# Kernel optimization log

Hardware: AMD Instinct MI355X
Metric: run time of the kernel (lower is better)

The kernel has to match this reference:

```python
import jax, jax.numpy as jnp
import numpy as np

N_HEADS = 16
ROPE = 64        # qk_rope_head_dim
KV_LORA = 512
V_DIM = 128
THETA = 10000.0

def rms_norm(x, w, eps=1e-6):
    return x * jax.lax.rsqrt(jnp.mean(x * x, axis=-1, keepdims=True) + eps) * w

def rope_cos_sin(T, d, theta=THETA):
    half = d // 2
    inv = 1.0 / theta ** (jnp.arange(half, dtype=jnp.float32) / half)
    ang = jnp.arange(T, dtype=jnp.float32)[:, None] * inv  # (T, half)
    return jnp.cos(ang), jnp.sin(ang)

def apply_rot(x, cos, sin):
    # x: (B,T,H,D); complex rotation on interleaved pairs
    xr, xi = x[..., 0::2], x[..., 1::2]
    c = cos[None, :, None, :]
    s = sin[None, :, None, :]
    orr = xr * c - xi * s
    oi = xr * s + xi * c
    return jnp.stack([orr, oi], axis=-1).reshape(x.shape)

def setup_inputs() -> dict:
    key = jax.random.key(0)
    ks = jax.random.split(key, 8)
    B, T, C = 2, 2048, 2048
    QLR = 1536
    x = jax.random.normal(ks[0], (B, T, C), dtype=jnp.float32)
    mask = jnp.tril(jnp.ones((T, T), dtype=jnp.int32))[None, None]
    sc = 0.02
    w_qa = jax.random.normal(ks[1], (QLR, C), dtype=jnp.float32) * sc
    qa_norm_w = jnp.ones((QLR,), dtype=jnp.float32)
    w_qb = jax.random.normal(ks[2], (N_HEADS * 2 * ROPE, QLR), dtype=jnp.float32) * sc
    w_kva = jax.random.normal(ks[3], (KV_LORA + ROPE, C), dtype=jnp.float32) * sc
    kva_norm_w = jnp.ones((KV_LORA,), dtype=jnp.float32)
    w_kvb = jax.random.normal(ks[4], (N_HEADS * (ROPE + V_DIM), KV_LORA), dtype=jnp.float32) * sc
    w_o = jax.random.normal(ks[5], (C, N_HEADS * V_DIM), dtype=jnp.float32) * sc
    return {"x": x, "mask": mask, "w_qa": w_qa, "qa_norm_w": qa_norm_w, "w_qb": w_qb,
            "w_kva": w_kva, "kva_norm_w": kva_norm_w, "w_kvb": w_kvb, "w_o": w_o}

def reference(x, mask, w_qa, qa_norm_w, w_qb, w_kva, kva_norm_w, w_kvb, w_o):
    B, T, C = x.shape
    # Q: low-rank compress -> norm -> up-project, split nope/rope halves
    q_c = rms_norm(x @ w_qa.T, qa_norm_w)
    q = (q_c @ w_qb.T).reshape(B, T, N_HEADS, 2 * ROPE)
    q_nope, q_rope = q[..., :ROPE], q[..., ROPE:]
    # KV: joint low-rank + shared rope key
    kv_a = x @ w_kva.T
    kv_c = rms_norm(kv_a[..., :KV_LORA], kva_norm_w)
    k_rope_raw = kv_a[..., KV_LORA:]                       # (B,T,ROPE)
    kv = (kv_c @ w_kvb.T).reshape(B, T, N_HEADS, ROPE + V_DIM)
    k_content, v = kv[..., :ROPE], kv[..., ROPE:]
    k_rope = jnp.broadcast_to(k_rope_raw[:, :, None, :], (B, T, N_HEADS, ROPE))
    cos, sin = rope_cos_sin(T, ROPE)
    q_rope = apply_rot(q_rope, cos, sin)
    k_rope = apply_rot(k_rope, cos, sin)
    q = jnp.concatenate([q_nope, q_rope], axis=-1)         # (B,T,H,2*ROPE)
    k = jnp.concatenate([k_content, k_rope], axis=-1)
    att = jnp.einsum('bqhd,bkhd->bhqk', q, k) * (ROPE ** -0.5)
    att = jnp.where(mask == 0, -jnp.inf, att)
    att = jax.nn.softmax(att, axis=-1)
    # source's nan-guard: uniform attention if any nan appeared
    att = jnp.where(jnp.any(jnp.isnan(att)), jnp.float32(1.0 / T), att)
    out = jnp.einsum('bhqk,bkhd->bqhd', att, v).reshape(B, T, N_HEADS * V_DIM)
    return out @ w_o.T
```

## Files before the change

kernel.cpp:

```cpp
#include <hip/hip_runtime.h>

typedef short bf16x8 __attribute__((ext_vector_type(8)));
typedef unsigned short u16x8 __attribute__((ext_vector_type(8)));
typedef unsigned short u16x4 __attribute__((ext_vector_type(4)));
typedef float f32x4 __attribute__((ext_vector_type(4)));
typedef unsigned u32x4 __attribute__((ext_vector_type(4)));
typedef unsigned u32x2 __attribute__((ext_vector_type(2)));

#define DEV static __device__ __forceinline__

DEV float bf2f(unsigned short u) { return __uint_as_float(((unsigned)u) << 16); }
DEV unsigned short f2bf(float f) {
  unsigned u = __float_as_uint(f);
  return (unsigned short)((u + 0x7fffu + ((u >> 16) & 1u)) >> 16);
}
DEV unsigned cvtpk(float lo, float hi) {
  unsigned r;
  asm("v_cvt_pk_bf16_f32 %0, %1, %2" : "=v"(r) : "v"(lo), "v"(hi));
  return r;
}
DEV void p32swap(unsigned& a, unsigned& b) {
  asm volatile("v_permlane32_swap_b32 %0, %1" : "+v"(a), "+v"(b));
}
DEV void p16swap(unsigned& a, unsigned& b) {
  asm volatile("v_permlane16_swap_b32 %0, %1" : "+v"(a), "+v"(b));
}

#define GLDS16(g, l)                                                                   \
  __builtin_amdgcn_global_load_lds((const __attribute__((address_space(1))) void*)(g), \
                                   (__attribute__((address_space(3))) void*)(l), 16, 0, 0)

__global__ __launch_bounds__(256) void convert_pad(const float* __restrict__ src,
                                                   unsigned short* __restrict__ dst,
                                                   int rows, int cols, int dstRows) {
  int i = blockIdx.x * 256 + threadIdx.x;
  int total4 = (dstRows * cols) >> 2;
  if (i >= total4) return;
  int e = i << 2;
  int r = e / cols;
  int c = e - r * cols;
  u16x4 o = {0, 0, 0, 0};
  if (r < rows) {
    const float* p = src + (size_t)r * cols + c;
    o[0] = f2bf(p[0]); o[1] = f2bf(p[1]); o[2] = f2bf(p[2]); o[3] = f2bf(p[3]);
  }
  *(u16x4*)(dst + e) = o;
}

template <typename OutT>
__global__ __launch_bounds__(256, 2) void gemm_bt(const unsigned short* __restrict__ A,
                                                  const unsigned short* __restrict__ B,
                                                  OutT* __restrict__ C, int M, int N, int K) {
  __shared__ __align__(16) unsigned short As[128 * 64];
  __shared__ __align__(16) unsigned short Bs[128 * 64];
  const int tid = threadIdx.x;
  const int lane = tid & 63, wave = tid >> 6;
  const int l16 = lane & 15, lhi = lane >> 4;
  const int nbn = N >> 7;
  const int bm = blockIdx.x / nbn, bn = blockIdx.x - bm * nbn;
  const int m0 = bm << 7, n0 = bn << 7;
  const int wm = (wave >> 1) << 6, wn = (wave & 1) << 6;
  f32x4 acc[4][4] = {};
  for (int k0 = 0; k0 < K; k0 += 64) {
#pragma unroll
    for (int it = 0; it < 4; ++it) {
      int slot = it * 256 + tid;
      int row = slot >> 3, col = (slot & 7) << 3;
      GLDS16(A + (size_t)(m0 + row) * K + k0 + col, As + (it * 256 + wave * 64) * 8);
      GLDS16(B + (size_t)(n0 + row) * K + k0 + col, Bs + (it * 256 + wave * 64) * 8);
    }
    __syncthreads();
#pragma unroll
    for (int ks = 0; ks < 2; ++ks) {
      bf16x8 a[4], b[4];
#pragma unroll
      for (int i = 0; i < 4; ++i) {
        a[i] = *(const bf16x8*)(As + (wm + i * 16 + l16) * 64 + ks * 32 + lhi * 8);
        b[i] = *(const bf16x8*)(Bs + (wn + i * 16 + l16) * 64 + ks * 32 + lhi * 8);
      }
#pragma unroll
      for (int i = 0; i < 4; ++i)
#pragma unroll
        for (int j = 0; j < 4; ++j)
          acc[i][j] = __builtin_amdgcn_mfma_f32_16x16x32_bf16(a[i], b[j], acc[i][j], 0, 0, 0);
    }
    __syncthreads();
  }
#pragma unroll
  for (int i = 0; i < 4; ++i)
#pragma unroll
    for (int j = 0; j < 4; ++j)
#pragma unroll
      for (int r = 0; r < 4; ++r) {
        int row = m0 + wm + i * 16 + lhi * 4 + r;
        int col = n0 + wn + j * 16 + l16;
        float v = acc[i][j][r];
        if constexpr (sizeof(OutT) == 4)
          C[(size_t)row * N + col] = v;
        else
          C[(size_t)row * N + col] = (OutT)f2bf(v);
      }
}

__global__ __launch_bounds__(256) void rms_q(const unsigned short* __restrict__ in,
                                             const float* __restrict__ w,
                                             unsigned short* __restrict__ out) {
  const int row = blockIdx.x, tid = threadIdx.x;
  const unsigned short* p = in + (size_t)row * 2176;
  float f[8];
  float ss = 0.f;
  const bool act = tid < 192;
  if (act) {
    u16x8 v = *(const u16x8*)(p + tid * 8);
#pragma unroll
    for (int j = 0; j < 8; ++j) { f[j] = bf2f(v[j]); ss += f[j] * f[j]; }
  }
#pragma unroll
  for (int m = 1; m <= 32; m <<= 1) ss += __shfl_xor(ss, m);
  __shared__ float red[4];
  if ((tid & 63) == 0) red[tid >> 6] = ss;
  __syncthreads();
  float rstd = rsqrtf((red[0] + red[1] + red[2] + red[3]) * (1.f / 1536.f) + 1e-6f);
  if (act) {
    u16x8 o;
#pragma unroll
    for (int j = 0; j < 8; ++j) o[j] = f2bf(f[j] * rstd * w[tid * 8 + j]);
    *(u16x8*)(out + (size_t)row * 1536 + tid * 8) = o;
  }
}

__global__ __launch_bounds__(256) void rms_kv(const unsigned short* __restrict__ qkva,
                                              const float* __restrict__ w,
                                              unsigned short* __restrict__ kvc,
                                              unsigned short* __restrict__ krope) {
  const int row = blockIdx.x, tid = threadIdx.x;
  const unsigned short* p = qkva + (size_t)row * 2176 + 1536;
  float f0 = bf2f(p[tid * 2]), f1 = bf2f(p[tid * 2 + 1]);
  float ss = f0 * f0 + f1 * f1;
#pragma unroll
  for (int m = 1; m <= 32; m <<= 1) ss += __shfl_xor(ss, m);
  __shared__ float red[4];
  if ((tid & 63) == 0) red[tid >> 6] = ss;
  __syncthreads();
  float rstd = rsqrtf((red[0] + red[1] + red[2] + red[3]) * (1.f / 512.f) + 1e-6f);
  kvc[(size_t)row * 512 + tid * 2]     = f2bf(f0 * rstd * w[tid * 2]);
  kvc[(size_t)row * 512 + tid * 2 + 1] = f2bf(f1 * rstd * w[tid * 2 + 1]);
  if (tid < 32) {
    int j = tid;
    float xr = bf2f(p[512 + 2 * j]), xi = bf2f(p[512 + 2 * j + 1]);
    int t = row & 2047;
    float ang = (float)t * powf(10000.f, -(float)j * (1.f / 32.f));
    float c = cosf(ang), s = sinf(ang);
    krope[(size_t)row * 64 + 2 * j]     = f2bf(xr * c - xi * s);
    krope[(size_t)row * 64 + 2 * j + 1] = f2bf(xr * s + xi * c);
  }
}

__global__ __launch_bounds__(256) void kv_asm_k(const unsigned short* __restrict__ kvfull,
                                                const unsigned short* __restrict__ krope,
                                                unsigned short* __restrict__ K) {
  int i = blockIdx.x * 256 + threadIdx.x;
  if (i >= 2 * 2048 * 16 * 128) return;
  int d = i & 127, h = (i >> 7) & 15, tl = i >> 11;
  int b = tl >> 11, t = tl & 2047;
  size_t oidx = ((size_t)((b * 16 + h) * 2048 + t)) * 128 + d;
  K[oidx] = (d < 64) ? kvfull[(size_t)tl * 3072 + h * 192 + d] : krope[(size_t)tl * 64 + d - 64];
}

__global__ __launch_bounds__(256) void v_transpose(const unsigned short* __restrict__ kvfull,
                                                   unsigned short* __restrict__ VT) {
  __shared__ unsigned short tile[64][137];
  const int tid = threadIdx.x;
  const int tt = blockIdx.x & 31, h = (blockIdx.x >> 5) & 15, b = blockIdx.x >> 9;
  const int t0 = tt * 64;
#pragma unroll
  for (int it = 0; it < 4; ++it) {
    int s = it * 256 + tid;
    int r = s >> 4, c = (s & 15) << 3;
    u16x8 v = *(const u16x8*)(kvfull + (size_t)(b * 2048 + t0 + r) * 3072 + h * 192 + 64 + c);
    *(u16x8*)(&tile[r][c]) = v;
  }
  __syncthreads();
#pragma unroll
  for (int it = 0; it < 4; ++it) {
    int s = it * 256 + tid;
    int d = s >> 3, tc = (s & 7) << 3;
    u16x8 o;
#pragma unroll
    for (int j = 0; j < 8; ++j) o[j] = tile[tc + j][d];
    *(u16x8*)(VT + ((size_t)(b * 16 + h) * 128 + d) * 2048 + t0 + tc) = o;
  }
}

__global__ __launch_bounds__(256, 2) void flash_attn(const unsigned short* __restrict__ qfull,
                                                     const unsigned short* __restrict__ Kt,
                                                     const unsigned short* __restrict__ Vt,
                                                     unsigned short* __restrict__ out) {
  const int tid = threadIdx.x, lane = tid & 63, wave = tid >> 6;
  const int l16 = lane & 15, lhi = lane >> 4;
  const int pr = blockIdx.x & 15;
  const int h = (blockIdx.x >> 4) & 15;
  const int b = blockIdx.x >> 8;
  const int sA = pr, sB = 31 - pr;
  __shared__ __align__(16) unsigned short Ks[2][64 * 128];
  __shared__ __align__(16) unsigned short Vs[2][64 * 128];

  bf16x8 qf[2][4];
  float m_run[2], l_run[2];
  int qrow_g[2];
  f32x4 o_acc[2][8] = {};
#pragma unroll
  for (int u = 0; u < 2; ++u) {
    const int s_u = u ? sB : sA;
    int t = s_u * 64 + wave * 16 + l16;
    qrow_g[u] = t;
    const unsigned short* qrow = qfull + (size_t)(b * 2048 + t) * 2048 + h * 128;
#pragma unroll
    for (int ks = 0; ks < 4; ++ks) {
      u16x8 raw = *(const u16x8*)(qrow + ks * 32 + lhi * 8);
      float f[8];
#pragma unroll
      for (int j = 0; j < 8; ++j) f[j] = bf2f(raw[j]);
      if (ks >= 2) {
#pragma unroll
        for (int pp = 0; pp < 4; ++pp) {
          int d = ks * 32 + lhi * 8 + 2 * pp;
          int jl = (d - 64) >> 1;
          float ang = (float)t * powf(10000.f, -(float)jl * (1.f / 32.f));
          float c = cosf(ang), s = sinf(ang);
          float xr = f[2 * pp], xi = f[2 * pp + 1];
          f[2 * pp] = xr * c - xi * s;
          f[2 * pp + 1] = xr * s + xi * c;
        }
      }
      bf16x8 fr;
#pragma unroll
      for (int j = 0; j < 8; ++j) fr[j] = (short)f2bf(f[j] * 0.125f);
      qf[u][ks] = fr;
    }
    m_run[u] = -1e30f;
    l_run[u] = 0.f;
  }

  const unsigned short* Kbh = Kt + (size_t)(b * 16 + h) * 2048 * 128;
  const unsigned short* Vbh = Vt + (size_t)(b * 16 + h) * 128 * 2048;

  auto stageK = [&](int kt, int buf) {
#pragma unroll
    for (int it = 0; it < 4; ++it) {
      int L = it * 4096 + wave * 1024 + lane * 16;
      int r = L >> 8;
      int w = (L & 255) ^ ((r & 7) << 4);
      GLDS16(Kbh + (size_t)(kt * 64 + r) * 128 + (w >> 1), &Ks[buf][(it * 4096 + wave * 1024) >> 1]);
    }
  };
  auto stageV = [&](int kt, int buf) {
#pragma unroll
    for (int it = 0; it < 4; ++it) {
      int L = it * 4096 + wave * 1024 + lane * 16;
      int d = L >> 7;
      int w = (L & 127) ^ ((d & 7) << 4);
      GLDS16(Vbh + (size_t)d * 2048 + kt * 64 + (w >> 1), &Vs[buf][(it * 4096 + wave * 1024) >> 1]);
    }
  };

  stageK(0, 0);
  stageV(0, 0);
  __syncthreads();
  int cur = 0;

  for (int kt = 0; kt <= sB; ++kt) {
    if (kt < sB) { stageK(kt + 1, cur ^ 1); stageV(kt + 1, cur ^ 1); }
    const unsigned short* Kb = Ks[cur];
    const unsigned short* Vb = Vs[cur];
    const bool actA = (kt <= sA);

    f32x4 st[2][4] = {};
    __builtin_amdgcn_s_setprio(1);
#pragma unroll
    for (int ks = 0; ks < 4; ++ks) {
      bf16x8 kf[4];
#pragma unroll
      for (int nt = 0; nt < 4; ++nt) {
        int row = nt * 16 + l16;
        int byteoff = row * 256 + ((ks * 64 + lhi * 16) ^ ((l16 & 7) << 4));
        kf[nt] = *(const bf16x8*)((const char*)Kb + byteoff);
      }
#pragma unroll
      for (int u = 0; u < 2; ++u) {
        if (u == 0 && !actA) continue;
#pragma unroll
        for (int nt = 0; nt < 4; ++nt)
          st[u][nt] = __builtin_amdgcn_mfma_f32_16x16x32_bf16(kf[nt], qf[u][ks], st[u][nt], 0, 0, 0);
      }
    }
    __builtin_amdgcn_s_setprio(0);

    bf16x8 pw[2][2];
#pragma unroll
    for (int u = 0; u < 2; ++u) {
      if (u == 0 && !actA) continue;
      const int s_u = u ? sB : sA;
      if (kt == s_u) {
#pragma unroll
        for (int nt = 0; nt < 4; ++nt)
#pragma unroll
          for (int r = 0; r < 4; ++r) {
            int kg = kt * 64 + nt * 16 + lhi * 4 + r;
            st[u][nt][r] = (kg <= qrow_g[u]) ? st[u][nt][r] : -1e30f;
          }
      }
      float mx = -1e30f;
#pragma unroll
      for (int nt = 0; nt < 4; ++nt)
#pragma unroll
        for (int r = 0; r < 4; ++r) mx = fmaxf(mx, st[u][nt][r]);
      mx = fmaxf(mx, __shfl_xor(mx, 16));
      mx = fmaxf(mx, __shfl_xor(mx, 32));
      float mnew = fmaxf(m_run[u], mx);
      float sc = __expf(m_run[u] - mnew);
      m_run[u] = mnew;
      float sum = 0.f;
#pragma unroll
      for (int nt = 0; nt < 4; ++nt)
#pragma unroll
        for (int r = 0; r < 4; ++r) {
          float p = __expf(st[u][nt][r] - mnew);
          st[u][nt][r] = p;
          sum += p;
        }
      sum += __shfl_xor(sum, 16);
      sum += __shfl_xor(sum, 32);
      l_run[u] = l_run[u] * sc + sum;
#pragma unroll
      for (int dt = 0; dt < 8; ++dt) o_acc[u][dt] *= sc;
      unsigned pk01[4], pk23[4];
#pragma unroll
      for (int nt = 0; nt < 4; ++nt) {
        pk01[nt] = cvtpk(st[u][nt][0], st[u][nt][1]);
        pk23[nt] = cvtpk(st[u][nt][2], st[u][nt][3]);
      }
#pragma unroll
      for (int k2 = 0; k2 < 2; ++k2) {
        unsigned a0 = pk01[2 * k2], b0 = pk01[2 * k2 + 1];
        unsigned a1 = pk23[2 * k2], b1 = pk23[2 * k2 + 1];
        p32swap(a0, b0); p16swap(a0, b0);
        p32swap(a1, b1); p16swap(a1, b1);
        u32x4 t4 = {a0, a1, b0, b1};
        pw[u][k2] = *(bf16x8*)&t4;
      }
    }

    __builtin_amdgcn_s_setprio(1);
#pragma unroll
    for (int k2 = 0; k2 < 2; ++k2)
#pragma unroll
      for (int dt = 0; dt < 8; ++dt) {
        int row = dt * 16 + l16;
        int byteoff = row * 128 + ((k2 * 64 + lhi * 16) ^ ((l16 & 7) << 4));
        bf16x8 vf = *(const bf16x8*)((const char*)Vb + byteoff);
#pragma unroll
        for (int u = 0; u < 2; ++u) {
          if (u == 0 && !actA) continue;
          o_acc[u][dt] = __builtin_amdgcn_mfma_f32_16x16x32_bf16(vf, pw[u][k2], o_acc[u][dt], 0, 0, 0);
        }
      }
    __builtin_amdgcn_s_setprio(0);

    __syncthreads();
    cur ^= 1;
  }

#pragma unroll
  for (int u = 0; u < 2; ++u) {
    float inv = 1.0f / l_run[u];
    unsigned short* orow = out + (size_t)(b * 2048 + qrow_g[u]) * 2048 + h * 128;
#pragma unroll
    for (int dt = 0; dt < 8; ++dt) {
      unsigned w01 = cvtpk(o_acc[u][dt][0] * inv, o_acc[u][dt][1] * inv);
      unsigned w23 = cvtpk(o_acc[u][dt][2] * inv, o_acc[u][dt][3] * inv);
      u32x2 st2 = {w01, w23};
      *(u32x2*)(orow + dt * 16 + lhi * 4) = st2;
    }
  }
}

extern "C" void kernel_launch(void* const* d_in, const int* in_sizes, int n_in,
                              void* d_out, int out_size, void* d_ws, size_t ws_size,
                              hipStream_t stream) {
  (void)in_sizes; (void)n_in; (void)out_size; (void)ws_size;
  const float* x      = (const float*)d_in[0];
  const float* w_qa   = (const float*)d_in[2];
  const float* qa_nw  = (const float*)d_in[3];
  const float* w_qb   = (const float*)d_in[4];
  const float* w_kva  = (const float*)d_in[5];
  const float* kva_nw = (const float*)d_in[6];
  const float* w_kvb  = (const float*)d_in[7];
  const float* w_o    = (const float*)d_in[8];
  float* out = (float*)d_out;
  char* ws = (char*)d_ws;

  unsigned short* xb     = (unsigned short*)(ws + 0);
  unsigned short* wqkva  = (unsigned short*)(ws + 16777216);
  unsigned short* wqbb   = (unsigned short*)(ws + 25690112);
  unsigned short* wkvbb  = (unsigned short*)(ws + 31981568);
  unsigned short* wob    = (unsigned short*)(ws + 35127296);
  unsigned short* qkva   = (unsigned short*)(ws + 43515904);
  unsigned short* qfull  = (unsigned short*)(ws + 43515904);
  unsigned short* q_c    = (unsigned short*)(ws + 61341696);
  unsigned short* kv_c   = (unsigned short*)(ws + 73924608);
  unsigned short* krope  = (unsigned short*)(ws + 78118912);
  unsigned short* attno  = (unsigned short*)(ws + 61341696);
  unsigned short* Vattn  = (unsigned short*)(ws + 78643200);
  unsigned short* Kattn  = xb;
  unsigned short* kvfull = (unsigned short*)d_out;

  convert_pad<<<8192, 256, 0, stream>>>(x,     xb,    4096, 2048, 4096);
  convert_pad<<<3072, 256, 0, stream>>>(w_qa,  wqkva, 1536, 2048, 1536);
  convert_pad<<<1280, 256, 0, stream>>>(w_kva, wqkva + (size_t)1536 * 2048, 576, 2048, 640);
  convert_pad<<<3072, 256, 0, stream>>>(w_qb,  wqbb,  2048, 1536, 2048);
  convert_pad<<<1536, 256, 0, stream>>>(w_kvb, wkvbb, 3072,  512, 3072);
  convert_pad<<<4096, 256, 0, stream>>>(w_o,   wob,   2048, 2048, 2048);

  gemm_bt<unsigned short><<<32 * 17, 256, 0, stream>>>(xb, wqkva, qkva, 4096, 2176, 2048);

  rms_q<<<4096, 256, 0, stream>>>(qkva, qa_nw, q_c);
  rms_kv<<<4096, 256, 0, stream>>>(qkva, kva_nw, kv_c, krope);

  gemm_bt<unsigned short><<<32 * 16, 256, 0, stream>>>(q_c,  wqbb,  qfull,  4096, 2048, 1536);
  gemm_bt<unsigned short><<<32 * 24, 256, 0, stream>>>(kv_c, wkvbb, kvfull, 4096, 3072,  512);

  kv_asm_k<<<32768, 256, 0, stream>>>(kvfull, krope, Kattn);
  v_transpose<<<1024, 256, 0, stream>>>(kvfull, Vattn);

  flash_attn<<<512, 256, 0, stream>>>(qfull, Kattn, Vattn, attno);

  gemm_bt<float><<<32 * 16, 256, 0, stream>>>(attno, wob, out, 4096, 2048, 2048);
}
```

Baseline: 310.8 us.

## Fuse conversions and RMS norms, drop K assembly, add lazy softmax rescale

Merges the six fp32-to-bf16 conversion launches into one kernel and the two RMS-norm kernels into one. Removes the separate K-assembly kernel: flash attention now gathers K directly from the kv projection output and the rotated rope buffer during its LDS staging. Flash attention also folds log2(e) into the Q scale so it can use exp2f, skips the running-max rescale unless the max grows by more than 8, and remaps block indices so work is spread across XCDs. This cuts launches and an extra write and read of K, at the cost of strided gathers in the attention loads.

```diff
diff --git a/kernel.cpp b/kernel.cpp
--- a/kernel.cpp
+++ b/kernel.cpp
@@ -30,12 +30,9 @@
   __builtin_amdgcn_global_load_lds((const __attribute__((address_space(1))) void*)(g), \
                                    (__attribute__((address_space(3))) void*)(l), 16, 0, 0)
 
-__global__ __launch_bounds__(256) void convert_pad(const float* __restrict__ src,
-                                                   unsigned short* __restrict__ dst,
-                                                   int rows, int cols, int dstRows) {
-  int i = blockIdx.x * 256 + threadIdx.x;
-  int total4 = (dstRows * cols) >> 2;
-  if (i >= total4) return;
+DEV void cvt_body(const float* __restrict__ src, unsigned short* __restrict__ dst,
+                  int rows, int cols, int dstRows, int bid) {
+  int i = bid * 256 + (int)threadIdx.x;
   int e = i << 2;
   int r = e / cols;
   int c = e - r * cols;
@@ -45,6 +42,21 @@
     o[0] = f2bf(p[0]); o[1] = f2bf(p[1]); o[2] = f2bf(p[2]); o[3] = f2bf(p[3]);
   }
   *(u16x4*)(dst + e) = o;
+}
+
+__global__ __launch_bounds__(256) void convert_all(
+    const float* __restrict__ x, const float* __restrict__ w_qa, const float* __restrict__ w_kva,
+    const float* __restrict__ w_qb, const float* __restrict__ w_kvb, const float* __restrict__ w_o,
+    unsigned short* __restrict__ xb, unsigned short* __restrict__ wqkva,
+    unsigned short* __restrict__ wqbb, unsigned short* __restrict__ wkvbb,
+    unsigned short* __restrict__ wob) {
+  int bid = blockIdx.x;
+  if (bid < 8192)        cvt_body(x,     xb,                        4096, 2048, 4096, bid);
+  else if (bid < 11264)  cvt_body(w_qa,  wqkva,                     1536, 2048, 1536, bid - 8192);
+  else if (bid < 12544)  cvt_body(w_kva, wqkva + (size_t)1536*2048,  576, 2048,  640, bid - 11264);
+  else if (bid < 15616)  cvt_body(w_qb,  wqbb,                      2048, 1536, 2048, bid - 12544);
+  else if (bid < 17152)  cvt_body(w_kvb, wkvbb,                     3072,  512, 3072, bid - 15616);
+  else                   cvt_body(w_o,   wob,                       2048, 2048, 2048, bid - 17152);
 }
 
 template <typename OutT>
@@ -102,69 +114,51 @@
       }
 }
 
-__global__ __launch_bounds__(256) void rms_q(const unsigned short* __restrict__ in,
-                                             const float* __restrict__ w,
-                                             unsigned short* __restrict__ out) {
+__global__ __launch_bounds__(256) void rms_fused(const unsigned short* __restrict__ qkva,
+                                                 const float* __restrict__ qw,
+                                                 const float* __restrict__ kvw,
+                                                 unsigned short* __restrict__ q_c,
+                                                 unsigned short* __restrict__ kv_c,
+                                                 unsigned short* __restrict__ krope) {
   const int row = blockIdx.x, tid = threadIdx.x;
-  const unsigned short* p = in + (size_t)row * 2176;
-  float f[8];
-  float ss = 0.f;
+  const unsigned short* p = qkva + (size_t)row * 2176;
+  float fq[8];
+  float ssq = 0.f;
   const bool act = tid < 192;
   if (act) {
     u16x8 v = *(const u16x8*)(p + tid * 8);
 #pragma unroll
-    for (int j = 0; j < 8; ++j) { f[j] = bf2f(v[j]); ss += f[j] * f[j]; }
-  }
-#pragma unroll
-  for (int m = 1; m <= 32; m <<= 1) ss += __shfl_xor(ss, m);
-  __shared__ float red[4];
-  if ((tid & 63) == 0) red[tid >> 6] = ss;
+    for (int j = 0; j < 8; ++j) { fq[j] = bf2f(v[j]); ssq += fq[j] * fq[j]; }
+  }
+  float f0 = bf2f(p[1536 + tid * 2]), f1 = bf2f(p[1536 + tid * 2 + 1]);
+  float sskv = f0 * f0 + f1 * f1;
+#pragma unroll
+  for (int m = 1; m <= 32; m <<= 1) {
+    ssq += __shfl_xor(ssq, m);
+    sskv += __shfl_xor(sskv, m);
+  }
+  __shared__ float rq[4], rkv[4];
+  if ((tid & 63) == 0) { rq[tid >> 6] = ssq; rkv[tid >> 6] = sskv; }
   __syncthreads();
-  float rstd = rsqrtf((red[0] + red[1] + red[2] + red[3]) * (1.f / 1536.f) + 1e-6f);
+  float rstdq = rsqrtf((rq[0] + rq[1] + rq[2] + rq[3]) * (1.f / 1536.f) + 1e-6f);
+  float rstdkv = rsqrtf((rkv[0] + rkv[1] + rkv[2] + rkv[3]) * (1.f / 512.f) + 1e-6f);
   if (act) {
     u16x8 o;
 #pragma unroll
-    for (int j = 0; j < 8; ++j) o[j] = f2bf(f[j] * rstd * w[tid * 8 + j]);
-    *(u16x8*)(out + (size_t)row * 1536 + tid * 8) = o;
-  }
-}
-
-__global__ __launch_bounds__(256) void rms_kv(const unsigned short* __restrict__ qkva,
-                                              const float* __restrict__ w,
-                                              unsigned short* __restrict__ kvc,
-                                              unsigned short* __restrict__ krope) {
-  const int row = blockIdx.x, tid = threadIdx.x;
-  const unsigned short* p = qkva + (size_t)row * 2176 + 1536;
-  float f0 = bf2f(p[tid * 2]), f1 = bf2f(p[tid * 2 + 1]);
-  float ss = f0 * f0 + f1 * f1;
-#pragma unroll
-  for (int m = 1; m <= 32; m <<= 1) ss += __shfl_xor(ss, m);
-  __shared__ float red[4];
-  if ((tid & 63) == 0) red[tid >> 6] = ss;
-  __syncthreads();
-  float rstd = rsqrtf((red[0] + red[1] + red[2] + red[3]) * (1.f / 512.f) + 1e-6f);
-  kvc[(size_t)row * 512 + tid * 2]     = f2bf(f0 * rstd * w[tid * 2]);
-  kvc[(size_t)row * 512 + tid * 2 + 1] = f2bf(f1 * rstd * w[tid * 2 + 1]);
+    for (int j = 0; j < 8; ++j) o[j] = f2bf(fq[j] * rstdq * qw[tid * 8 + j]);
+    *(u16x8*)(q_c + (size_t)row * 1536 + tid * 8) = o;
+  }
+  kv_c[(size_t)row * 512 + tid * 2]     = f2bf(f0 * rstdkv * kvw[tid * 2]);
+  kv_c[(size_t)row * 512 + tid * 2 + 1] = f2bf(f1 * rstdkv * kvw[tid * 2 + 1]);
   if (tid < 32) {
     int j = tid;
-    float xr = bf2f(p[512 + 2 * j]), xi = bf2f(p[512 + 2 * j + 1]);
+    float xr = bf2f(p[2048 + 2 * j]), xi = bf2f(p[2048 + 2 * j + 1]);
     int t = row & 2047;
     float ang = (float)t * powf(10000.f, -(float)j * (1.f / 32.f));
     float c = cosf(ang), s = sinf(ang);
     krope[(size_t)row * 64 + 2 * j]     = f2bf(xr * c - xi * s);
     krope[(size_t)row * 64 + 2 * j + 1] = f2bf(xr * s + xi * c);
   }
-}
-
-__global__ __launch_bounds__(256) void kv_asm_k(const unsigned short* __restrict__ kvfull,
-                                                const unsigned short* __restrict__ krope,
-                                                unsigned short* __restrict__ K) {
-  int i = blockIdx.x * 256 + threadIdx.x;
-  if (i >= 2 * 2048 * 16 * 128) return;
-  int d = i & 127, h = (i >> 7) & 15, tl = i >> 11;
-  int b = tl >> 11, t = tl & 2047;
-  size_t oidx = ((size_t)((b * 16 + h) * 2048 + t)) * 128 + d;
-  K[oidx] = (d < 64) ? kvfull[(size_t)tl * 3072 + h * 192 + d] : krope[(size_t)tl * 64 + d - 64];
 }
 
 __global__ __launch_bounds__(256) void v_transpose(const unsigned short* __restrict__ kvfull,
@@ -193,18 +187,22 @@
 }
 
 __global__ __launch_bounds__(256, 2) void flash_attn(const unsigned short* __restrict__ qfull,
-                                                     const unsigned short* __restrict__ Kt,
+                                                     const unsigned short* __restrict__ kvfull,
+                                                     const unsigned short* __restrict__ krope,
                                                      const unsigned short* __restrict__ Vt,
                                                      unsigned short* __restrict__ out) {
   const int tid = threadIdx.x, lane = tid & 63, wave = tid >> 6;
   const int l16 = lane & 15, lhi = lane >> 4;
-  const int pr = blockIdx.x & 15;
-  const int h = (blockIdx.x >> 4) & 15;
-  const int b = blockIdx.x >> 8;
+  const int bid = blockIdx.x;
+  const int vid = (bid & 7) * 64 + (bid >> 3);
+  const int pr = vid & 15;
+  const int h = (vid >> 4) & 15;
+  const int b = vid >> 8;
   const int sA = pr, sB = 31 - pr;
   __shared__ __align__(16) unsigned short Ks[2][64 * 128];
   __shared__ __align__(16) unsigned short Vs[2][64 * 128];
 
+  const float QSCALE = 0.125f * 1.44269504089f;
   bf16x8 qf[2][4];
   float m_run[2], l_run[2];
   int qrow_g[2];
@@ -235,14 +233,14 @@
       }
       bf16x8 fr;
 #pragma unroll
-      for (int j = 0; j < 8; ++j) fr[j] = (short)f2bf(f[j] * 0.125f);
+      for (int j = 0; j < 8; ++j) fr[j] = (short)f2bf(f[j] * QSCALE);
       qf[u][ks] = fr;
     }
     m_run[u] = -1e30f;
     l_run[u] = 0.f;
   }
 
-  const unsigned short* Kbh = Kt + (size_t)(b * 16 + h) * 2048 * 128;
+  const int bT = b * 2048;
   const unsigned short* Vbh = Vt + (size_t)(b * 16 + h) * 128 * 2048;
 
   auto stageK = [&](int kt, int buf) {
@@ -251,7 +249,11 @@
       int L = it * 4096 + wave * 1024 + lane * 16;
       int r = L >> 8;
       int w = (L & 255) ^ ((r & 7) << 4);
-      GLDS16(Kbh + (size_t)(kt * 64 + r) * 128 + (w >> 1), &Ks[buf][(it * 4096 + wave * 1024) >> 1]);
+      int c = w >> 1;
+      int tl = bT + kt * 64 + r;
+      const unsigned short* src = (c < 64) ? kvfull + (size_t)tl * 3072 + h * 192 + c
+                                           : krope + (size_t)tl * 64 + (c - 64);
+      GLDS16(src, &Ks[buf][(it * 4096 + wave * 1024) >> 1]);
     }
   };
   auto stageV = [&](int kt, int buf) {
@@ -317,23 +319,27 @@
         for (int r = 0; r < 4; ++r) mx = fmaxf(mx, st[u][nt][r]);
       mx = fmaxf(mx, __shfl_xor(mx, 16));
       mx = fmaxf(mx, __shfl_xor(mx, 32));
-      float mnew = fmaxf(m_run[u], mx);
-      float sc = __expf(m_run[u] - mnew);
-      m_run[u] = mnew;
+      if (__ballot(mx > m_run[u] + 8.f)) {
+        float mnew = fmaxf(m_run[u], mx);
+        float sc = exp2f(m_run[u] - mnew);
+        m_run[u] = mnew;
+        l_run[u] *= sc;
+#pragma unroll
+        for (int dt = 0; dt < 8; ++dt) o_acc[u][dt] *= sc;
+      }
+      const float mcur = m_run[u];
       float sum = 0.f;
 #pragma unroll
       for (int nt = 0; nt < 4; ++nt)
 #pragma unroll
         for (int r = 0; r < 4; ++r) {
-          float p = __expf(st[u][nt][r] - mnew);
+          float p = exp2f(st[u][nt][r] - mcur);
           st[u][nt][r] = p;
           sum += p;
         }
       sum += __shfl_xor(sum, 16);
       sum += __shfl_xor(sum, 32);
-      l_run[u] = l_run[u] * sc + sum;
-#pragma unroll
-      for (int dt = 0; dt < 8; ++dt) o_acc[u][dt] *= sc;
+      l_run[u] += sum;
       unsigned pk01[4], pk23[4];
 #pragma unroll
       for (int nt = 0; nt < 4; ++nt) {
@@ -412,28 +418,21 @@
   unsigned short* krope  = (unsigned short*)(ws + 78118912);
   unsigned short* attno  = (unsigned short*)(ws + 61341696);
   unsigned short* Vattn  = (unsigned short*)(ws + 78643200);
-  unsigned short* Kattn  = xb;
   unsigned short* kvfull = (unsigned short*)d_out;
 
-  convert_pad<<<8192, 256, 0, stream>>>(x,     xb,    4096, 2048, 4096);
-  convert_pad<<<3072, 256, 0, stream>>>(w_qa,  wqkva, 1536, 2048, 1536);
-  convert_pad<<<1280, 256, 0, stream>>>(w_kva, wqkva + (size_t)1536 * 2048, 576, 2048, 640);
-  convert_pad<<<3072, 256, 0, stream>>>(w_qb,  wqbb,  2048, 1536, 2048);
-  convert_pad<<<1536, 256, 0, stream>>>(w_kvb, wkvbb, 3072,  512, 3072);
-  convert_pad<<<4096, 256, 0, stream>>>(w_o,   wob,   2048, 2048, 2048);
+  convert_all<<<21248, 256, 0, stream>>>(x, w_qa, w_kva, w_qb, w_kvb, w_o,
+                                         xb, wqkva, wqbb, wkvbb, wob);
 
   gemm_bt<unsigned short><<<32 * 17, 256, 0, stream>>>(xb, wqkva, qkva, 4096, 2176, 2048);
 
-  rms_q<<<4096, 256, 0, stream>>>(qkva, qa_nw, q_c);
-  rms_kv<<<4096, 256, 0, stream>>>(qkva, kva_nw, kv_c, krope);
+  rms_fused<<<4096, 256, 0, stream>>>(qkva, qa_nw, kva_nw, q_c, kv_c, krope);
 
   gemm_bt<unsigned short><<<32 * 16, 256, 0, stream>>>(q_c,  wqbb,  qfull,  4096, 2048, 1536);
   gemm_bt<unsigned short><<<32 * 24, 256, 0, stream>>>(kv_c, wkvbb, kvfull, 4096, 3072,  512);
 
-  kv_asm_k<<<32768, 256, 0, stream>>>(kvfull, krope, Kattn);
   v_transpose<<<1024, 256, 0, stream>>>(kvfull, Vattn);
 
-  flash_attn<<<512, 256, 0, stream>>>(qfull, Kattn, Vattn, attno);
+  flash_attn<<<512, 256, 0, stream>>>(qfull, kvfull, krope, Vattn, attno);
 
   gemm_bt<float><<<32 * 16, 256, 0, stream>>>(attno, wob, out, 4096, 2048, 2048);
 }
```

Result: faster. 286.6 us (-7.8%).
